# Performance work log

Measured on AMD Instinct MI355X. Metric: run time of the kernel, lower is better.

## Reference

```python
import jax, jax.numpy as jnp
import numpy as np

NUM_SITES_X = 2048
NUM_SITES_Y = 4096
NUM_CLB_SITES = 6_000_000
NUM_SLICE_SITES = 6_000_000
NUM_SITES = NUM_SITES_X * NUM_SITES_Y  # global flattened site-id space


def setup_inputs() -> dict:
    key = jax.random.key(0)
    k1, k2, k3, k4 = jax.random.split(key, 4)
    # CLB slice site ids (x*num_sites_y + y), sorted as produced from the column-major fabric scan
    slice_sites = jnp.sort(
        jax.random.randint(k1, (NUM_SLICE_SITES,), 0, NUM_SITES, dtype=jnp.int32))
    # per-CLB-site signature count; >0 means the site already has instances committed
    site_det_sig_idx = jax.random.randint(
        k2, (NUM_CLB_SITES,), 0, 4, dtype=jnp.int32)
    # compact CLB address -> global site id map (monotone by construction in the original)
    addr2site_map = jnp.sort(
        jax.random.randint(k3, (NUM_CLB_SITES,), 0, NUM_SITES, dtype=jnp.int32))
    # per-slice-site legalization score (site_det_score analogue)
    site_scores = jax.random.normal(k4, (NUM_SLICE_SITES,), dtype=jnp.float32)
    return {
        "slice_sites": slice_sites,
        "site_det_sig_idx": site_det_sig_idx,
        "addr2site_map": addr2site_map,
        "site_scores": site_scores,
    }


def _remaining_mask(slice_sites, site_det_sig_idx, addr2site_map):
    """Faithful jit-friendly version of compute_remaining_slice_sites.

    torch/np original:
      assigned = addr2site_map[site_det_sig_idx > 0]
      mask[np.in1d(slice_sites, assigned)] = True; return ~mask
    We avoid the data-dependent boolean gather by replacing unassigned
    entries with a -1 sentinel (site ids are >= 0), sorting, and doing a
    vectorized membership test via searchsorted.
    """
    n = addr2site_map.shape[0]
    assigned = jnp.where(site_det_sig_idx > 0, addr2site_map, jnp.int32(-1))
    assigned_sorted = jnp.sort(assigned)  # sentinels land at the front
    pos = jnp.searchsorted(assigned_sorted, slice_sites, side="left")
    pos = jnp.clip(pos, 0, n - 1)
    found = assigned_sorted[pos] == slice_sites  # in1d membership
    return ~found  # True where the slice site is still available


def reference(slice_sites, site_det_sig_idx, addr2site_map, site_scores):
    remaining = _remaining_mask(slice_sites, site_det_sig_idx, addr2site_map)
    # scores of still-available candidate sites (zeros where already assigned)
    avail_scores = jnp.where(remaining, site_scores, jnp.zeros((), site_scores.dtype))
    return remaining, avail_scores
```

## Files before the change

### kernel.cpp

```cpp
#include <hip/hip_runtime.h>


typedef int   v4i __attribute__((ext_vector_type(4)));
typedef float v4f __attribute__((ext_vector_type(4)));

static constexpr int NUM_SITES_TOTAL = 2048 * 4096;
static constexpr int WORDS_PER_BLOCK = 128;
static constexpr int SITES_PER_BLOCK = WORDS_PER_BLOCK * 32;
static constexpr int GRID            = NUM_SITES_TOTAL / SITES_PER_BLOCK;
static constexpr int BLOCK           = 256;

__global__ __launch_bounds__(BLOCK) void boundary_kernel(
    const int* __restrict__ ss, const int* __restrict__ a2s,
    int* __restrict__ eb, int* __restrict__ pb, int n_slice, int n_clb)
{
    const int g = blockIdx.x * BLOCK + threadIdx.x;
    if (g > GRID) return;
    const int key = g * SITES_PER_BLOCK;

    int lo = 0, hi = n_clb;
    while (lo < hi) { int m = (lo + hi) >> 1; if (a2s[m] < key) lo = m + 1; else hi = m; }
    eb[g] = lo;

    lo = 0; hi = n_slice;
    while (lo < hi) { int m = (lo + hi) >> 1; if (ss[m] < key) lo = m + 1; else hi = m; }
    pb[g] = lo;
}

__global__ __launch_bounds__(BLOCK) void fused_kernel(
    const int*   __restrict__ ss,
    const int*   __restrict__ sig,
    const int*   __restrict__ a2s,
    const float* __restrict__ sc,
    const int*   __restrict__ eb,
    const int*   __restrict__ pb,
    float*       __restrict__ rem,
    float*       __restrict__ avail,
    int n_clb)
{
    __shared__ unsigned int lbm[WORDS_PER_BLOCK];

    const int g        = blockIdx.x;
    const int siteBase = g * SITES_PER_BLOCK;
    const int siteEnd  = siteBase + SITES_PER_BLOCK;

    for (int w = threadIdx.x; w < WORDS_PER_BLOCK; w += BLOCK) lbm[w] = 0u;

    const int e0 = eb[g], e1 = eb[g + 1];
    const int p0 = pb[g], p1 = pb[g + 1];

    __syncthreads();

    const int mstart = e0 & ~3;
    for (int s = mstart + threadIdx.x * 4; s < e1; s += BLOCK * 4) {
        int av[4], gv[4];
        if (s + 4 <= n_clb) {
            v4i a = __builtin_nontemporal_load((const v4i*)(a2s + s));
            v4i gg = __builtin_nontemporal_load((const v4i*)(sig + s));
            av[0]=a.x; av[1]=a.y; av[2]=a.z; av[3]=a.w;
            gv[0]=gg.x; gv[1]=gg.y; gv[2]=gg.z; gv[3]=gg.w;
        } else {
#pragma unroll
            for (int j = 0; j < 4; ++j) {
                const int i = s + j;
                const bool ok = i < n_clb;
                av[j] = ok ? a2s[i] : -1;
                gv[j] = ok ? sig[i] : 0;
            }
        }
        unsigned int curw = 0xFFFFFFFFu, curm = 0u;
#pragma unroll
        for (int j = 0; j < 4; ++j) {
            const int site = av[j];
            if (gv[j] > 0 && site >= siteBase && site < siteEnd) {
                const unsigned int u = (unsigned int)(site - siteBase);
                const unsigned int w = u >> 5;
                const unsigned int m = 1u << (u & 31u);
                if (w == curw) curm |= m;
                else { if (curm) atomicOr(&lbm[curw], curm); curw = w; curm = m; }
            }
        }
        if (curm) atomicOr(&lbm[curw], curm);
    }

    __syncthreads();

    int i0 = (p0 + 3) & ~3;
    int i1 = p1 & ~3;
    if (i1 < i0) i1 = i0;

    for (int q = (i0 >> 2) + threadIdx.x; q < (i1 >> 2); q += BLOCK) {
        v4i s = __builtin_nontemporal_load((const v4i*)ss + q);
        v4f f = __builtin_nontemporal_load((const v4f*)sc + q);
        v4f r, a;
#pragma unroll
        for (int j = 0; j < 4; ++j) {
            const unsigned int u   = (unsigned int)(s[j] - siteBase);
            const unsigned int bit = (lbm[u >> 5] >> (u & 31u)) & 1u;
            r[j] = bit ? 0.0f : 1.0f;
            a[j] = bit ? 0.0f : f[j];
        }
        __builtin_nontemporal_store(r, (v4f*)rem + q);
        __builtin_nontemporal_store(a, (v4f*)avail + q);
    }
    for (int i = p0 + threadIdx.x; i < min(i0, p1); i += BLOCK) {
        const unsigned int u   = (unsigned int)(ss[i] - siteBase);
        const unsigned int bit = (lbm[u >> 5] >> (u & 31u)) & 1u;
        rem[i]   = bit ? 0.0f : 1.0f;
        avail[i] = bit ? 0.0f : sc[i];
    }
    for (int i = max(i1, p0) + threadIdx.x; i < p1; i += BLOCK) {
        const unsigned int u   = (unsigned int)(ss[i] - siteBase);
        const unsigned int bit = (lbm[u >> 5] >> (u & 31u)) & 1u;
        rem[i]   = bit ? 0.0f : 1.0f;
        avail[i] = bit ? 0.0f : sc[i];
    }
}

extern "C" void kernel_launch(void* const* d_in, const int* in_sizes, int n_in,
                              void* d_out, int out_size, void* d_ws, size_t ws_size,
                              hipStream_t stream) {
    const int*   slice_sites = (const int*)d_in[0];
    const int*   sig         = (const int*)d_in[1];
    const int*   a2s         = (const int*)d_in[2];
    const float* scores      = (const float*)d_in[3];
    const int n_slice = in_sizes[0];
    const int n_clb   = in_sizes[1];

    int* eb = (int*)d_ws;
    int* pb = eb + (GRID + 1);

    boundary_kernel<<<(GRID + 1 + BLOCK - 1) / BLOCK, BLOCK, 0, stream>>>(
        slice_sites, a2s, eb, pb, n_slice, n_clb);

    float* rem   = (float*)d_out;
    float* avail = rem + n_slice;

    fused_kernel<<<GRID, BLOCK, 0, stream>>>(
        slice_sites, sig, a2s, scores, eb, pb, rem, avail, n_clb);
}
```

Baseline: 157.5 us.

## Compute bin boundaries by scanning sorted arrays for transitions instead of binary search

The per-bin binary searches are replaced by a full streaming pass over both sorted arrays, where each element writes boundary indices for every bin it crosses. The fused kernel also processes 8 CLB entries per thread per iteration instead of 4, issuing two vector loads per array. The boundary pass now reads all 12M entries (about 48MB) rather than doing roughly 2049 log-depth searches. That pass is likely more expensive than the latency-bound searches it replaces.

```diff
diff --git a/kernel.cpp b/kernel.cpp
--- a/kernel.cpp
+++ b/kernel.cpp
@@ -4,27 +4,45 @@
 typedef int   v4i __attribute__((ext_vector_type(4)));
 typedef float v4f __attribute__((ext_vector_type(4)));
 
-static constexpr int NUM_SITES_TOTAL = 2048 * 4096;
 static constexpr int WORDS_PER_BLOCK = 128;
-static constexpr int SITES_PER_BLOCK = WORDS_PER_BLOCK * 32;
-static constexpr int GRID            = NUM_SITES_TOTAL / SITES_PER_BLOCK;
+static constexpr int SITES_PER_BLOCK = 4096;
+static constexpr int BIN_SHIFT       = 12;
+static constexpr int GRID            = 2048;
 static constexpr int BLOCK           = 256;
 
-__global__ __launch_bounds__(BLOCK) void boundary_kernel(
+__device__ __forceinline__ void transitions(
+    const int* __restrict__ x, int* __restrict__ bnd, int n, int t)
+{
+    const int s = t * 4;
+    if (s >= n) return;
+    int v[4];
+    int cnt;
+    if (s + 4 <= n) {
+        v4i a = __builtin_nontemporal_load((const v4i*)(x + s));
+        v[0] = a.x; v[1] = a.y; v[2] = a.z; v[3] = a.w;
+        cnt = 4;
+    } else {
+        cnt = n - s;
+        for (int j = 0; j < cnt; ++j) v[j] = x[s + j];
+    }
+    int pbin = (s == 0) ? -1 : (x[s - 1] >> BIN_SHIFT);
+    for (int j = 0; j < cnt; ++j) {
+        const int i = s + j;
+        const int cbin = v[j] >> BIN_SHIFT;
+        for (int b = pbin + 1; b <= cbin; ++b) bnd[b] = i;
+        if (i == n - 1)
+            for (int b = cbin + 1; b <= GRID; ++b) bnd[b] = n;
+        pbin = cbin;
+    }
+}
+
+__global__ __launch_bounds__(BLOCK) void bounds_kernel(
     const int* __restrict__ ss, const int* __restrict__ a2s,
-    int* __restrict__ eb, int* __restrict__ pb, int n_slice, int n_clb)
+    int* __restrict__ pb, int* __restrict__ eb, int n_slice, int n_clb)
 {
-    const int g = blockIdx.x * BLOCK + threadIdx.x;
-    if (g > GRID) return;
-    const int key = g * SITES_PER_BLOCK;
-
-    int lo = 0, hi = n_clb;
-    while (lo < hi) { int m = (lo + hi) >> 1; if (a2s[m] < key) lo = m + 1; else hi = m; }
-    eb[g] = lo;
-
-    lo = 0; hi = n_slice;
-    while (lo < hi) { int m = (lo + hi) >> 1; if (ss[m] < key) lo = m + 1; else hi = m; }
-    pb[g] = lo;
+    const int t = blockIdx.x * BLOCK + threadIdx.x;
+    transitions(ss,  pb, n_slice, t);
+    transitions(a2s, eb, n_clb,  t);
 }
 
 __global__ __launch_bounds__(BLOCK) void fused_kernel(
@@ -52,16 +70,20 @@
     __syncthreads();
 
     const int mstart = e0 & ~3;
-    for (int s = mstart + threadIdx.x * 4; s < e1; s += BLOCK * 4) {
-        int av[4], gv[4];
-        if (s + 4 <= n_clb) {
-            v4i a = __builtin_nontemporal_load((const v4i*)(a2s + s));
-            v4i gg = __builtin_nontemporal_load((const v4i*)(sig + s));
-            av[0]=a.x; av[1]=a.y; av[2]=a.z; av[3]=a.w;
-            gv[0]=gg.x; gv[1]=gg.y; gv[2]=gg.z; gv[3]=gg.w;
+    for (int s = mstart + threadIdx.x * 8; s < e1; s += BLOCK * 8) {
+        int av[8], gv[8];
+        if (s + 8 <= n_clb) {
+            v4i a0 = __builtin_nontemporal_load((const v4i*)(a2s + s));
+            v4i a1 = __builtin_nontemporal_load((const v4i*)(a2s + s + 4));
+            v4i g0 = __builtin_nontemporal_load((const v4i*)(sig + s));
+            v4i g1 = __builtin_nontemporal_load((const v4i*)(sig + s + 4));
+            av[0]=a0.x; av[1]=a0.y; av[2]=a0.z; av[3]=a0.w;
+            av[4]=a1.x; av[5]=a1.y; av[6]=a1.z; av[7]=a1.w;
+            gv[0]=g0.x; gv[1]=g0.y; gv[2]=g0.z; gv[3]=g0.w;
+            gv[4]=g1.x; gv[5]=g1.y; gv[6]=g1.z; gv[7]=g1.w;
         } else {
 #pragma unroll
-            for (int j = 0; j < 4; ++j) {
+            for (int j = 0; j < 8; ++j) {
                 const int i = s + j;
                 const bool ok = i < n_clb;
                 av[j] = ok ? a2s[i] : -1;
@@ -70,7 +92,7 @@
         }
         unsigned int curw = 0xFFFFFFFFu, curm = 0u;
 #pragma unroll
-        for (int j = 0; j < 4; ++j) {
+        for (int j = 0; j < 8; ++j) {
             const int site = av[j];
             if (gv[j] > 0 && site >= siteBase && site < siteEnd) {
                 const unsigned int u = (unsigned int)(site - siteBase);
@@ -130,8 +152,10 @@
     int* eb = (int*)d_ws;
     int* pb = eb + (GRID + 1);
 
-    boundary_kernel<<<(GRID + 1 + BLOCK - 1) / BLOCK, BLOCK, 0, stream>>>(
-        slice_sites, a2s, eb, pb, n_slice, n_clb);
+    const int n_max = n_slice > n_clb ? n_slice : n_clb;
+    const int tblocks = (n_max / 4 + BLOCK - 1) / BLOCK + 1;
+    bounds_kernel<<<tblocks, BLOCK, 0, stream>>>(
+        slice_sites, a2s, pb, eb, n_slice, n_clb);
 
     float* rem   = (float*)d_out;
     float* avail = rem + n_slice;
```

Result: faster. 150.0 us (-4.8%).
